# Kernel tuning notes

Measured on AMD Instinct MI355X. Metric: run time of the kernel, lower is better.

The kernel has to match this reference:

```python
import jax, jax.numpy as jnp
import numpy as np

N_NODES = 50000
N_EDGES = 800000
N_FEAT = 100
N_CLASSES = 40
K_HOPS = 2


def setup_inputs() -> dict:
    key = jax.random.key(0)
    k1, k2, k3, k4 = jax.random.split(key, 4)
    x = jax.random.normal(k1, (N_NODES, N_FEAT), dtype=jnp.float32)
    edge_index = jax.random.randint(k2, (2, N_EDGES), 0, N_NODES, dtype=jnp.int64)
    # linear layer params (PyG Linear: x @ W^T + b); store W as [F, C] for x @ W
    W = jax.random.normal(k3, (N_FEAT, N_CLASSES), dtype=jnp.float32) / np.sqrt(N_FEAT)
    b = jax.random.normal(k4, (N_CLASSES,), dtype=jnp.float32) * 0.01
    return {"x": x, "edge_index": edge_index, "W": W, "b": b}


def _gcn_norm(edge_index, num_nodes):
    # add self-loops with weight 1, compute symmetric normalization D^-1/2 A D^-1/2
    loop = jnp.arange(num_nodes, dtype=edge_index.dtype)
    row = jnp.concatenate([edge_index[0], loop])  # source
    col = jnp.concatenate([edge_index[1], loop])  # target
    w = jnp.ones(row.shape[0], dtype=jnp.float32)
    deg = jax.ops.segment_sum(w, col, num_segments=num_nodes)
    dinv = jnp.where(deg > 0, jax.lax.rsqrt(jnp.maximum(deg, 1.0)), 0.0)
    norm = dinv[row] * dinv[col]  # [E + N]
    return row, col, norm


def reference(x, edge_index, W, b):
    n = x.shape[0]
    row, col, norm = _gcn_norm(edge_index, n)
    # K-hop propagation: gather at source, scale, scatter-add at target
    h = x
    for _ in range(K_HOPS):
        msg = norm[:, None] * h[row]          # [E+N, F] edge-wise gather + scale
        h = jax.ops.segment_sum(msg, col, num_segments=n)  # scatter-add
    logits = h @ W + b                        # [N, C]
    return jax.nn.log_softmax(logits, axis=1)
```

## Files before the change

kernel.cpp:

```cpp
#include <hip/hip_runtime.h>
#include <hip/hip_fp16.h>
#include <hip/hip_fp8.h>
#include <math.h>

#define N_NODES 50000
#define N_EDGES 800000
#define N_FEAT 100
#define N_CLASSES 40
#define ROWB 64
#define N_SLICES 8
#define SLICE_NODES 6250
#define N_CHUNKS 125
#define EPC 6400
#define CF_BLOCKS (N_SLICES * N_CHUNKS)
#define SCAN_BLK 256
#define N_SCAN_BLKS 196
#define PAD 8
#define CONV_UNITS 3125
#define LIN_UNITS 1954
#define ZERO_UNITS 1173
#define N_SUPER 391
#define CL_BLOCKS (N_SUPER * 16)
#define CSR_ALLOC_ENTRIES (ZERO_UNITS * 256 * 4)


__device__ __forceinline__ unsigned char f2q(float x) {
    __hip_fp8_e4m3 q(x);
    return (unsigned char)q.__x;
}
#if __has_builtin(__builtin_amdgcn_cvt_f32_fp8)
__device__ __forceinline__ float q2f(unsigned int b) {
    return __builtin_amdgcn_cvt_f32_fp8((int)b, 0);
}
#else
__device__ __forceinline__ float q2f(unsigned int b) {
    __hip_fp8_e4m3 q;
    q.__x = (__hip_fp8_storage_t)(b & 0xffu);
    return (float)q;
}
#endif


__global__ void k_conv_lin(const void* __restrict__ ei,
                           unsigned int* __restrict__ epack,
                           const float* __restrict__ x, const float* __restrict__ W,
                           unsigned char* __restrict__ y0q, unsigned int* __restrict__ csr) {
    __shared__ float4 Ws[N_CLASSES / 4][N_FEAT + 1];
    int super = blockIdx.x >> 4;
    int pos = blockIdx.x & 15;
    if (pos < 8) {
        int unit = super * 8 + pos;
        if (unit >= CONV_UNITS) return;
        int e = unit * 256 + threadIdx.x;
        long long v = __builtin_nontemporal_load((const long long*)ei + e);
        bool bad = (v < 0 || v >= N_NODES);
        bool is32 = (__ballot(bad) != 0ull);
        unsigned int r, c;
        if (is32) {
            const unsigned int* p = (const unsigned int*)ei;
            r = __builtin_nontemporal_load(p + e);
            c = __builtin_nontemporal_load(p + N_EDGES + e);
        } else {
            r = (unsigned int)v;
            c = (unsigned int)__builtin_nontemporal_load((const long long*)ei + N_EDGES + e);
        }
        epack[e] = r | (c << 16);
    } else if (pos < 13) {
        int unit = super * 5 + (pos - 8);
        if (unit >= LIN_UNITS) return;
        for (int i = threadIdx.x; i < N_FEAT * (N_CLASSES / 4); i += blockDim.x) {
            int k = i / (N_CLASSES / 4), c4 = i - k * (N_CLASSES / 4);
            Ws[c4][k] = ((const float4*)W)[i];
        }
        __syncthreads();
        int idx = unit * 256 + threadIdx.x;
        if (idx >= N_NODES * (N_CLASSES / 4)) return;
        int n = idx / (N_CLASSES / 4);
        int c4 = idx - n * (N_CLASSES / 4);
        const float* hr = x + (size_t)n * N_FEAT;
        float4 s = {0.f, 0.f, 0.f, 0.f};
#pragma unroll
        for (int k = 0; k < N_FEAT; ++k) {
            float hv = hr[k];
            float4 w = Ws[c4][k];
            s.x += hv * w.x; s.y += hv * w.y; s.z += hv * w.z; s.w += hv * w.w;
        }
        uchar4 q = make_uchar4(f2q(s.x), f2q(s.y), f2q(s.z), f2q(s.w));
        *(uchar4*)(y0q + (size_t)n * ROWB + c4 * 4) = q;
    } else {
        int unit = super * 3 + (pos - 13);
        if (unit >= ZERO_UNITS) return;
        ((uint4*)csr)[unit * 256 + threadIdx.x] = make_uint4(0u, 0u, 0u, 0u);
    }
}


__global__ void k_count(const unsigned int* __restrict__ epack, unsigned short* __restrict__ dp) {
    __shared__ int hist[SLICE_NODES];
    int slice = blockIdx.x & (N_SLICES - 1);
    int chunk = blockIdx.x >> 3;
    unsigned int lo = slice * SLICE_NODES;
    for (int i = threadIdx.x; i < SLICE_NODES; i += blockDim.x) hist[i] = 0;
    __syncthreads();
    int g0 = chunk * (EPC / 4), g1 = g0 + (EPC / 4);
    for (int g = g0 + threadIdx.x; g < g1; g += blockDim.x) {
        uint4 p4 = ((const uint4*)epack)[g];
        unsigned int c0 = p4.x >> 16, c1 = p4.y >> 16, c2 = p4.z >> 16, c3 = p4.w >> 16;
        if (c0 - lo < SLICE_NODES) atomicAdd(&hist[c0 - lo], 1);
        if (c1 - lo < SLICE_NODES) atomicAdd(&hist[c1 - lo], 1);
        if (c2 - lo < SLICE_NODES) atomicAdd(&hist[c2 - lo], 1);
        if (c3 - lo < SLICE_NODES) atomicAdd(&hist[c3 - lo], 1);
    }
    __syncthreads();
    unsigned short* dpk = dp + (size_t)chunk * N_NODES + lo;
    for (int i = threadIdx.x; i < SLICE_NODES; i += blockDim.x) dpk[i] = (unsigned short)hist[i];
}


__global__ void k_scan1(unsigned short* __restrict__ dp, int* __restrict__ offs,
                        int* __restrict__ sums, float* __restrict__ dinv,
                        unsigned short* __restrict__ dinv16) {
    __shared__ int s[SCAN_BLK];
    int i = blockIdx.x * SCAN_BLK + threadIdx.x;
    int padded = 0;
    if (i < N_NODES) {
        int run = 0;
#pragma unroll 5
        for (int k = 0; k < N_CHUNKS; ++k) {
            unsigned short* p = dp + (size_t)k * N_NODES + i;
            int t = *p;
            *p = (unsigned short)run;
            run += t;
        }
        float d = rsqrtf((float)run + 1.0f);
        dinv[i] = d;
        dinv16[i] = __half_as_ushort(__float2half_rn(d));
        padded = (run + PAD - 1) & ~(PAD - 1);
    }
    s[threadIdx.x] = padded;
    __syncthreads();
    int v = s[threadIdx.x];
    for (int off = 1; off < SCAN_BLK; off <<= 1) {
        int t = (threadIdx.x >= off) ? s[threadIdx.x - off] : 0;
        __syncthreads();
        s[threadIdx.x] += t;
        __syncthreads();
    }
    if (i < N_NODES) offs[i] = s[threadIdx.x] - v;
    if (threadIdx.x == SCAN_BLK - 1) sums[blockIdx.x] = s[SCAN_BLK - 1];
}

__global__ void k_scan3(int* __restrict__ offs, const int* __restrict__ sums) {
    __shared__ int sc[SCAN_BLK];
    __shared__ int orig[SCAN_BLK];
    int t = threadIdx.x;
    int v = (t < N_SCAN_BLKS) ? sums[t] : 0;
    sc[t] = v; orig[t] = v;
    __syncthreads();
    for (int off = 1; off < SCAN_BLK; off <<= 1) {
        int u = (t >= off) ? sc[t - off] : 0;
        __syncthreads();
        sc[t] += u;
        __syncthreads();
    }
    int base = sc[blockIdx.x] - orig[blockIdx.x];
    int i = blockIdx.x * SCAN_BLK + t;
    if (i < N_NODES) offs[i] += base;
    if (blockIdx.x == 0 && t == N_SCAN_BLKS - 1) offs[N_NODES] = sc[t];
}


__global__ void k_fill(const unsigned int* __restrict__ epack,
                       const unsigned short* __restrict__ dinv16,
                       const int* __restrict__ offs, const unsigned short* __restrict__ dp,
                       unsigned int* __restrict__ csr) {
    __shared__ int pos[SLICE_NODES];
    int slice = blockIdx.x & (N_SLICES - 1);
    int chunk = blockIdx.x >> 3;
    unsigned int lo = slice * SLICE_NODES;
    const unsigned short* dpk = dp + (size_t)chunk * N_NODES + lo;
    const int* ofs = offs + lo;
    for (int i = threadIdx.x; i < SLICE_NODES; i += blockDim.x)
        pos[i] = ofs[i] + dpk[i];
    __syncthreads();
    int g0 = chunk * (EPC / 4), g1 = g0 + (EPC / 4);
    for (int g = g0 + threadIdx.x; g < g1; g += blockDim.x) {
        uint4 p4 = ((const uint4*)epack)[g];
#pragma unroll
        for (int j = 0; j < 4; ++j) {
            unsigned int p = (j == 0) ? p4.x : (j == 1) ? p4.y : (j == 2) ? p4.z : p4.w;
            unsigned int c = p >> 16;
            if (c - lo < SLICE_NODES) {
                unsigned int r = p & 0xffffu;
                int pp = atomicAdd(&pos[c - lo], 1);
                csr[pp] = r | ((unsigned int)dinv16[r] << 16);
            }
        }
    }
}


#define GPROC(Q, ACC)                                                            \
    {                                                                            \
        unsigned int q_ = (Q);                                                   \
        float vv_ = q2f(sl[(size_t)(q_ & 0xffffu) * ROWB]);                      \
        ACC += __half2float(__ushort_as_half((unsigned short)(q_ >> 16))) * vv_; \
    }

template <bool LSM, typename DstT, int DSTRIDE>
__global__ void k_gather(const int* __restrict__ offs, const unsigned int* __restrict__ csr,
                         const unsigned char* __restrict__ src, const float* __restrict__ dinv,
                         DstT* __restrict__ dst, const float* __restrict__ bias) {
    int wave = threadIdx.x >> 6;
    int lane = threadIdx.x & 63;
    int n = blockIdx.x * 4 + wave;
    if (n >= N_NODES) return;
    int s = offs[n], e = offs[n + 1];
    bool act = (lane < N_CLASSES);
    float dc = dinv[n];
    const unsigned char* sl = src + lane;
    float acc0 = 0.0f, acc1 = 0.0f, acc2 = 0.0f, acc3 = 0.0f;
    if (act) acc0 = dc * q2f(sl[(size_t)n * ROWB]);
    int base = s;
    for (; base + 16 <= e; base += 16) {
        uint4 a0 = *(const uint4*)(csr + base);
        uint4 a1 = *(const uint4*)(csr + base + 4);
        uint4 a2 = *(const uint4*)(csr + base + 8);
        uint4 a3 = *(const uint4*)(csr + base + 12);
        if (act) {
            GPROC(a0.x, acc0) GPROC(a0.y, acc1) GPROC(a0.z, acc2) GPROC(a0.w, acc3)
            GPROC(a1.x, acc0) GPROC(a1.y, acc1) GPROC(a1.z, acc2) GPROC(a1.w, acc3)
            GPROC(a2.x, acc0) GPROC(a2.y, acc1) GPROC(a2.z, acc2) GPROC(a2.w, acc3)
            GPROC(a3.x, acc0) GPROC(a3.y, acc1) GPROC(a3.z, acc2) GPROC(a3.w, acc3)
        }
    }
    if (base < e) {
        uint4 a0 = *(const uint4*)(csr + base);
        uint4 a1 = *(const uint4*)(csr + base + 4);
        if (act) {
            GPROC(a0.x, acc0) GPROC(a0.y, acc1) GPROC(a0.z, acc2) GPROC(a0.w, acc3)
            GPROC(a1.x, acc0) GPROC(a1.y, acc1) GPROC(a1.z, acc2) GPROC(a1.w, acc3)
        }
    }
    float acc = dc * ((acc0 + acc1) + (acc2 + acc3));
    if (!LSM) {
        if (act) {
            if constexpr (sizeof(DstT) == 1)
                dst[(size_t)n * DSTRIDE + lane] = (DstT)f2q(acc);
            else
                dst[(size_t)n * DSTRIDE + lane] = (DstT)acc;
        }
    } else {
        float v = act ? acc + bias[lane] : -INFINITY;
        float m = v;
#pragma unroll
        for (int off = 32; off; off >>= 1) m = fmaxf(m, __shfl_xor(m, off));
        float ex = act ? __expf(v - m) : 0.0f;
        float ssum = ex;
#pragma unroll
        for (int off = 32; off; off >>= 1) ssum += __shfl_xor(ssum, off);
        float ls = logf(ssum);
        if (act) dst[(size_t)n * DSTRIDE + lane] = (DstT)(v - m - ls);
    }
}


extern "C" void kernel_launch(void* const* d_in, const int* in_sizes, int n_in,
                              void* d_out, int out_size, void* d_ws, size_t ws_size,
                              hipStream_t stream) {
    const float* x = (const float*)d_in[0];
    const void* ei = d_in[1];
    const float* W = (const float*)d_in[2];
    const float* b = (const float*)d_in[3];
    float* z = (float*)d_out;

    char* ws = (char*)d_ws;
    size_t o = 0;
    auto alloc = [&](size_t bytes) { char* p = ws + o; o += (bytes + 255) & ~(size_t)255; return p; };
    unsigned int*   epack  = (unsigned int*)alloc((size_t)N_EDGES * 4);
    unsigned short* dp     = (unsigned short*)alloc((size_t)N_CHUNKS * N_NODES * 2);
    float*          dinv   = (float*)alloc(N_NODES * 4);
    unsigned short* dinv16 = (unsigned short*)alloc(N_NODES * 2);
    int*            offs   = (int*)alloc((N_NODES + 1) * 4);
    int*            sums   = (int*)alloc(SCAN_BLK * 4);
    unsigned int*   csr    = (unsigned int*)alloc((size_t)CSR_ALLOC_ENTRIES * 4);
    unsigned char*  y0q    = (unsigned char*)alloc((size_t)N_NODES * ROWB);
    unsigned char*  h1q    = (unsigned char*)alloc((size_t)N_NODES * ROWB);

    const int T = 256;

    k_conv_lin<<<CL_BLOCKS, T, 0, stream>>>(ei, epack, x, W, y0q, csr);

    k_count<<<CF_BLOCKS, T, 0, stream>>>(epack, dp);

    k_scan1<<<N_SCAN_BLKS, SCAN_BLK, 0, stream>>>(dp, offs, sums, dinv, dinv16);
    k_scan3<<<N_SCAN_BLKS, SCAN_BLK, 0, stream>>>(offs, sums);

    k_fill<<<CF_BLOCKS, T, 0, stream>>>(epack, dinv16, offs, dp, csr);

    k_gather<false, unsigned char, ROWB><<<N_NODES / 4, T, 0, stream>>>(offs, csr, y0q, dinv, h1q, b);
    k_gather<true, float, N_CLASSES><<<N_NODES / 4, T, 0, stream>>>(offs, csr, h1q, dinv, z, b);
}
```

Before: 118.1 us.

## Fuse degree histogram into front kernel reading raw edge_index directly

Measured after the change: 125.6 us. 6.3% more time.

```diff
diff --git a/kernel.cpp b/kernel.cpp
--- a/kernel.cpp
+++ b/kernel.cpp
@@ -20,7 +20,7 @@
 #define LIN_UNITS 1954
 #define ZERO_UNITS 1173
 #define N_SUPER 391
-#define CL_BLOCKS (N_SUPER * 16)
+#define FRONT_BLOCKS (CF_BLOCKS + N_SUPER * 16)
 #define CSR_ALLOC_ENTRIES (ZERO_UNITS * 256 * 4)
 
 
@@ -41,13 +41,41 @@
 #endif
 
 
-__global__ void k_conv_lin(const void* __restrict__ ei,
-                           unsigned int* __restrict__ epack,
-                           const float* __restrict__ x, const float* __restrict__ W,
-                           unsigned char* __restrict__ y0q, unsigned int* __restrict__ csr) {
-    __shared__ float4 Ws[N_CLASSES / 4][N_FEAT + 1];
-    int super = blockIdx.x >> 4;
-    int pos = blockIdx.x & 15;
+__global__ void k_front(const void* __restrict__ ei,
+                        unsigned int* __restrict__ epack, unsigned short* __restrict__ dp,
+                        const float* __restrict__ x, const float* __restrict__ W,
+                        unsigned char* __restrict__ y0q, unsigned int* __restrict__ csr) {
+    __shared__ __align__(16) unsigned char smem[SLICE_NODES * 4];
+    if (blockIdx.x < CF_BLOCKS) {
+        int* hist = (int*)smem;
+        int slice = blockIdx.x & (N_SLICES - 1);
+        int chunk = blockIdx.x >> 3;
+        unsigned int lo = slice * SLICE_NODES;
+        for (int i = threadIdx.x; i < SLICE_NODES; i += blockDim.x) hist[i] = 0;
+        __syncthreads();
+        int e0 = chunk * EPC;
+        for (int k = 0; k < EPC / 256; ++k) {
+            int e = e0 + k * 256 + threadIdx.x;
+            long long v = ((const long long*)ei)[e];
+            bool bad = (v < 0 || v >= N_NODES);
+            bool is32 = (__ballot(bad) != 0ull);
+            unsigned int c;
+            if (is32) {
+                c = ((const unsigned int*)ei)[N_EDGES + e];
+            } else {
+                c = (unsigned int)((const long long*)ei)[N_EDGES + e];
+            }
+            if (c - lo < SLICE_NODES) atomicAdd(&hist[c - lo], 1);
+        }
+        __syncthreads();
+        unsigned short* dpk = dp + (size_t)chunk * N_NODES + lo;
+        for (int i = threadIdx.x; i < SLICE_NODES; i += blockDim.x)
+            dpk[i] = (unsigned short)hist[i];
+        return;
+    }
+    int rb = blockIdx.x - CF_BLOCKS;
+    int super = rb >> 4;
+    int pos = rb & 15;
     if (pos < 8) {
         int unit = super * 8 + pos;
         if (unit >= CONV_UNITS) return;
@@ -68,6 +96,7 @@
     } else if (pos < 13) {
         int unit = super * 5 + (pos - 8);
         if (unit >= LIN_UNITS) return;
+        float4 (*Ws)[N_FEAT + 1] = (float4(*)[N_FEAT + 1])smem;
         for (int i = threadIdx.x; i < N_FEAT * (N_CLASSES / 4); i += blockDim.x) {
             int k = i / (N_CLASSES / 4), c4 = i - k * (N_CLASSES / 4);
             Ws[c4][k] = ((const float4*)W)[i];
@@ -92,28 +121,6 @@
         if (unit >= ZERO_UNITS) return;
         ((uint4*)csr)[unit * 256 + threadIdx.x] = make_uint4(0u, 0u, 0u, 0u);
     }
-}
-
-
-__global__ void k_count(const unsigned int* __restrict__ epack, unsigned short* __restrict__ dp) {
-    __shared__ int hist[SLICE_NODES];
-    int slice = blockIdx.x & (N_SLICES - 1);
-    int chunk = blockIdx.x >> 3;
-    unsigned int lo = slice * SLICE_NODES;
-    for (int i = threadIdx.x; i < SLICE_NODES; i += blockDim.x) hist[i] = 0;
-    __syncthreads();
-    int g0 = chunk * (EPC / 4), g1 = g0 + (EPC / 4);
-    for (int g = g0 + threadIdx.x; g < g1; g += blockDim.x) {
-        uint4 p4 = ((const uint4*)epack)[g];
-        unsigned int c0 = p4.x >> 16, c1 = p4.y >> 16, c2 = p4.z >> 16, c3 = p4.w >> 16;
-        if (c0 - lo < SLICE_NODES) atomicAdd(&hist[c0 - lo], 1);
-        if (c1 - lo < SLICE_NODES) atomicAdd(&hist[c1 - lo], 1);
-        if (c2 - lo < SLICE_NODES) atomicAdd(&hist[c2 - lo], 1);
-        if (c3 - lo < SLICE_NODES) atomicAdd(&hist[c3 - lo], 1);
-    }
-    __syncthreads();
-    unsigned short* dpk = dp + (size_t)chunk * N_NODES + lo;
-    for (int i = threadIdx.x; i < SLICE_NODES; i += blockDim.x) dpk[i] = (unsigned short)hist[i];
 }
 
 
@@ -289,9 +296,7 @@
 
     const int T = 256;
 
-    k_conv_lin<<<CL_BLOCKS, T, 0, stream>>>(ei, epack, x, W, y0q, csr);
-
-    k_count<<<CF_BLOCKS, T, 0, stream>>>(epack, dp);
+    k_front<<<FRONT_BLOCKS, T, 0, stream>>>(ei, epack, dp, x, W, y0q, csr);
 
     k_scan1<<<N_SCAN_BLKS, SCAN_BLK, 0, stream>>>(dp, offs, sums, dinv, dinv16);
     k_scan3<<<N_SCAN_BLKS, SCAN_BLK, 0, stream>>>(offs, sums);
```
